# Optimization experiments

Hardware: AMD Instinct MI355X
Metric: run time of the kernel (lower is better)

The kernel has to match this reference:

```python
import jax, jax.numpy as jnp
import numpy as np

N, F, D, R, E = 1024, 256, 64, 11, 2048
ALPHA = 0.2  # LeakyReLU negative slope


def setup_inputs() -> dict:
    key = jax.random.key(0)
    k1, k2, k3, k4, k5, k6 = jax.random.split(key, 6)
    x = jax.random.normal(k1, (N, F), dtype=jnp.float32)
    # Relation-specific weights (ParameterList of [F, D]) stacked: [R, F, D]
    W = jax.random.normal(k2, (R, F, D), dtype=jnp.float32) * (1.414 * (6.0 / (F + D)) ** 0.5)
    # nn.Linear(2*D, 1, bias=False) weight as a vector [2*D]
    a = jax.random.normal(k3, (2 * D,), dtype=jnp.float32) * (1.0 / (2 * D) ** 0.5)
    src_idx = jax.random.randint(k4, (E,), 0, N, dtype=jnp.int32)
    dst_idx = jax.random.randint(k5, (E,), 0, N, dtype=jnp.int32)
    rel_idx = jax.random.randint(k6, (E,), 0, R, dtype=jnp.int32)
    return {"x": x, "W": W, "a": a, "src_idx": src_idx, "dst_idx": dst_idx, "rel_idx": rel_idx}


def reference(x, W, a, src_idx, dst_idx, rel_idx):
    # Per-edge relation weight gather: [E, F, D]
    We = W[rel_idx]
    # einsum('i,ij->ij', emb, W) == row-wise scaling of W by the embedding
    nt = x[dst_idx][:, :, None] * We          # neighbour_temp: [E, F, D]
    ft = x[src_idx][:, :, None] * We          # feature_temp:   [E, F, D]
    hh = jnp.concatenate([ft, nt], axis=-1)   # [E, F, 2D]
    # linear(2D -> 1, no bias) then LeakyReLU: [E, F]
    e = jax.nn.leaky_relu(jnp.einsum('efd,d->ef', hh, a), ALPHA)
    # original: attn = softmax over edge dim (dim=1 of [F, E]); here edges are axis 0
    attn = jax.nn.softmax(e, axis=0)          # [E, F]
    # h[e] = attn[:, e, None] * nt[e]; cat over edges along dim=1 then sum over F
    # => per edge: sum_F attn[e, f] * nt[e, f, :] -> [E, D], flattened to [E*D]
    out = jnp.einsum('ef,efd->ed', attn, nt).reshape(-1)
    return out
```

## Files before the change

### kernel.cpp

```cpp
#include <hip/hip_runtime.h>
#include <hip/hip_bf16.h>

#define NN 1024
#define FF 256
#define DD 64
#define RR 11
#define EE 2048
#define ALPHA 0.2f
#define TPB 512
#define EPT (EE / TPB)
#define TILE_E 32
#define PERM_CAP 2432
#define K2_GRID (PERM_CAP / TILE_E)


__global__ __launch_bounds__(TPB) void k1_coef(
    const float* __restrict__ x, const float* __restrict__ W,
    const float* __restrict__ a, const int* __restrict__ src,
    const int* __restrict__ dst, const int* __restrict__ rel,
    float* __restrict__ cbuf, int* __restrict__ perm,
    int* __restrict__ ntiles_p) {

    const int b    = blockIdx.x;
    const int f    = ((b & 7) << 5) | (b >> 3);
    const int tid  = threadIdx.x;
    const int wid  = tid >> 6;
    const int lane = tid & 63;

    __shared__ float xcol[NN];
    __shared__ float p_sh[RR], q_sh[RR];
    __shared__ float red_s[8];
    __shared__ int   hist[16], off_sh[16];

    for (int i = tid; i < NN; i += TPB) xcol[i] = x[(size_t)i * FF + f];

    for (int r = wid; r < RR; r += 8) {
        float w  = W[((size_t)r * FF + f) * DD + lane];
        float pa = w * a[lane];
        float qa = w * a[DD + lane];
        #pragma unroll
        for (int o = 32; o > 0; o >>= 1) {
            pa += __shfl_down(pa, o);
            qa += __shfl_down(qa, o);
        }
        if (lane == 0) { p_sh[r] = pa; q_sh[r] = qa; }
    }
    __syncthreads();

    float uvals[EPT];
    float s = 0.0f;
    #pragma unroll
    for (int k = 0; k < EPT; ++k) {
        int e = tid + k * TPB;
        float xs = xcol[src[e]];
        float xd = xcol[dst[e]];
        int r = rel[e];
        float v = xs * p_sh[r] + xd * q_sh[r];
        v = v > 0.0f ? v : ALPHA * v;
        float ev = expf(v);
        uvals[k] = ev * xd;
        s += ev;
    }
    #pragma unroll
    for (int o = 32; o > 0; o >>= 1) s += __shfl_down(s, o);
    if (lane == 0) red_s[wid] = s;
    __syncthreads();
    float st = red_s[0];
    #pragma unroll
    for (int i = 1; i < 8; ++i) st += red_s[i];
    float inv = 1.0f / st;

    #pragma unroll
    for (int k = 0; k < EPT; ++k) {
        int e = tid + k * TPB;
        cbuf[(size_t)e * FF + f] = uvals[k] * inv;
    }

    if (b == 0) {
        if (tid < 16) hist[tid] = 0;
        __syncthreads();
        for (int e = tid; e < EE; e += TPB) atomicAdd(&hist[rel[e]], 1);
        __syncthreads();
        if (tid == 0) {
            int acc = 0;
            for (int r = 0; r < RR; ++r) {
                off_sh[r] = acc;
                acc += (hist[r] + TILE_E - 1) & ~(TILE_E - 1);
            }
            *ntiles_p = acc / TILE_E;
        }
        __syncthreads();
        for (int i = tid; i < PERM_CAP; i += TPB) perm[i] = -1;
        __syncthreads();
        for (int e = tid; e < EE; e += TPB) {
            int pos = atomicAdd(&off_sh[rel[e]], 1);
            perm[pos] = e;
        }
    }
}

__global__ __launch_bounds__(TPB) void k2_out(
    const float* __restrict__ W, const int* __restrict__ rel,
    const float* __restrict__ cbuf, const int* __restrict__ perm,
    const int* __restrict__ ntiles_p, float* __restrict__ out) {

    const int t = blockIdx.x;
    if (t >= *ntiles_p) return;

    const int tid  = threadIdx.x;
    const int wid  = tid >> 6;
    const int lane = tid & 63;

    __shared__ float Wl[32 * DD];
    __shared__ int   e_sh[TILE_E];

    if (tid < TILE_E) e_sh[tid] = perm[t * TILE_E + tid];
    __syncthreads();

    const int r = rel[e_sh[0]];
    const float* __restrict__ Wr = W + (size_t)r * FF * DD;

    int eb[4];
    const float* ce[4];
    float4 acc[4];
    #pragma unroll
    for (int j = 0; j < 4; ++j) {
        eb[j]  = e_sh[wid * 4 + j];
        ce[j]  = cbuf + (size_t)(eb[j] >= 0 ? eb[j] : 0) * FF;
        acc[j] = make_float4(0.f, 0.f, 0.f, 0.f);
    }

    const int fg = lane >> 4;
    const int dq = lane & 15;
    const int srow = tid >> 4;
    const int scol = tid & 15;

    float4 nxt = *(const float4*)&Wr[(size_t)srow * DD + scol * 4];

    #pragma unroll
    for (int fc = 0; fc < FF / 32; ++fc) {
        __syncthreads();
        *(float4*)&Wl[srow * DD + scol * 4] = nxt;
        __syncthreads();
        if (fc < FF / 32 - 1)
            nxt = *(const float4*)
                &Wr[(size_t)((fc + 1) * 32 + srow) * DD + scol * 4];
        #pragma unroll
        for (int i = 0; i < 8; ++i) {
            int lf = i * 4 + fg;
            float4 w4 = *(const float4*)&Wl[lf * DD + dq * 4];
            int gf = fc * 32 + lf;
            #pragma unroll
            for (int j = 0; j < 4; ++j) {
                float c = ce[j][gf];
                acc[j].x = fmaf(c, w4.x, acc[j].x);
                acc[j].y = fmaf(c, w4.y, acc[j].y);
                acc[j].z = fmaf(c, w4.z, acc[j].z);
                acc[j].w = fmaf(c, w4.w, acc[j].w);
            }
        }
    }

    #pragma unroll
    for (int j = 0; j < 4; ++j) {
        #pragma unroll
        for (int o = 16; o <= 32; o <<= 1) {
            acc[j].x += __shfl_xor(acc[j].x, o);
            acc[j].y += __shfl_xor(acc[j].y, o);
            acc[j].z += __shfl_xor(acc[j].z, o);
            acc[j].w += __shfl_xor(acc[j].w, o);
        }
        if (eb[j] >= 0 && fg == 0)
            *(float4*)&out[(size_t)eb[j] * DD + dq * 4] = acc[j];
    }
}

extern "C" void kernel_launch(void* const* d_in, const int* in_sizes, int n_in,
                              void* d_out, int out_size, void* d_ws, size_t ws_size,
                              hipStream_t stream) {
    const float* x  = (const float*)d_in[0];
    const float* W  = (const float*)d_in[1];
    const float* a  = (const float*)d_in[2];
    const int* src  = (const int*)d_in[3];
    const int* dst  = (const int*)d_in[4];
    const int* rel  = (const int*)d_in[5];
    float* out      = (float*)d_out;

    char* wsb = (char*)d_ws;
    int*   ntiles_p = (int*)wsb;
    int*   perm     = (int*)(wsb + 256);
    float* cbuf     = (float*)(wsb + 16384);

    k1_coef<<<FF, TPB, 0, stream>>>(x, W, a, src, dst, rel,
                                    cbuf, perm, ntiles_p);
    k2_out<<<K2_GRID, TPB, 0, stream>>>(W, rel, cbuf, perm, ntiles_p, out);
}
```

Baseline: 21.68 us.

## Process four features per block in coefficient kernel and split perm build into own block

Each k1 block now handles four adjacent feature columns, loading x rows as float4 and reusing the src/dst/rel indices held in registers across all four. The permutation-building work moves from block 0 into a dedicated extra block so it no longer delays one compute block. The aim is to cut redundant index loads and strided gathers of x. In exchange the grid shrinks from 256 to 65 blocks on a GPU with many CUs, which lowers parallelism.

Result: slower. 25.95 us (+19.7%).

```diff
diff --git a/kernel.cpp b/kernel.cpp
--- a/kernel.cpp
+++ b/kernel.cpp
@@ -9,6 +9,8 @@
 #define ALPHA 0.2f
 #define TPB 512
 #define EPT (EE / TPB)
+#define FB 4
+#define K1_GRID (FF / FB + 1)
 #define TILE_E 32
 #define PERM_CAP 2432
 #define K2_GRID (PERM_CAP / TILE_E)
@@ -22,61 +24,13 @@
     int* __restrict__ ntiles_p) {
 
     const int b    = blockIdx.x;
-    const int f    = ((b & 7) << 5) | (b >> 3);
     const int tid  = threadIdx.x;
     const int wid  = tid >> 6;
     const int lane = tid & 63;
 
-    __shared__ float xcol[NN];
-    __shared__ float p_sh[RR], q_sh[RR];
-    __shared__ float red_s[8];
-    __shared__ int   hist[16], off_sh[16];
-
-    for (int i = tid; i < NN; i += TPB) xcol[i] = x[(size_t)i * FF + f];
-
-    for (int r = wid; r < RR; r += 8) {
-        float w  = W[((size_t)r * FF + f) * DD + lane];
-        float pa = w * a[lane];
-        float qa = w * a[DD + lane];
-        #pragma unroll
-        for (int o = 32; o > 0; o >>= 1) {
-            pa += __shfl_down(pa, o);
-            qa += __shfl_down(qa, o);
-        }
-        if (lane == 0) { p_sh[r] = pa; q_sh[r] = qa; }
-    }
-    __syncthreads();
-
-    float uvals[EPT];
-    float s = 0.0f;
-    #pragma unroll
-    for (int k = 0; k < EPT; ++k) {
-        int e = tid + k * TPB;
-        float xs = xcol[src[e]];
-        float xd = xcol[dst[e]];
-        int r = rel[e];
-        float v = xs * p_sh[r] + xd * q_sh[r];
-        v = v > 0.0f ? v : ALPHA * v;
-        float ev = expf(v);
-        uvals[k] = ev * xd;
-        s += ev;
-    }
-    #pragma unroll
-    for (int o = 32; o > 0; o >>= 1) s += __shfl_down(s, o);
-    if (lane == 0) red_s[wid] = s;
-    __syncthreads();
-    float st = red_s[0];
-    #pragma unroll
-    for (int i = 1; i < 8; ++i) st += red_s[i];
-    float inv = 1.0f / st;
-
-    #pragma unroll
-    for (int k = 0; k < EPT; ++k) {
-        int e = tid + k * TPB;
-        cbuf[(size_t)e * FF + f] = uvals[k] * inv;
-    }
-
-    if (b == 0) {
+    __shared__ int hist[16], off_sh[16];
+
+    if (b == FF / FB) {
         if (tid < 16) hist[tid] = 0;
         __syncthreads();
         for (int e = tid; e < EE; e += TPB) atomicAdd(&hist[rel[e]], 1);
@@ -95,6 +49,71 @@
         for (int e = tid; e < EE; e += TPB) {
             int pos = atomicAdd(&off_sh[rel[e]], 1);
             perm[pos] = e;
+        }
+        return;
+    }
+
+    const int f0 = (((b & 7) << 3) | (b >> 3)) * FB;
+
+    __shared__ float xs[FB][NN];
+    __shared__ float p_sh[FB][RR], q_sh[FB][RR];
+    __shared__ float red_s[8];
+
+    #pragma unroll
+    for (int i = 0; i < NN / TPB; ++i) {
+        int row = tid + i * TPB;
+        float4 v = *(const float4*)&x[(size_t)row * FF + f0];
+        xs[0][row] = v.x; xs[1][row] = v.y; xs[2][row] = v.z; xs[3][row] = v.w;
+    }
+
+    for (int task = wid; task < FB * RR; task += 8) {
+        int ff = task & (FB - 1), r = task >> 2;
+        float wv = W[((size_t)r * FF + f0 + ff) * DD + lane];
+        float pa = wv * a[lane];
+        float qa = wv * a[DD + lane];
+        #pragma unroll
+        for (int o = 32; o > 0; o >>= 1) {
+            pa += __shfl_down(pa, o);
+            qa += __shfl_down(qa, o);
+        }
+        if (lane == 0) { p_sh[ff][r] = pa; q_sh[ff][r] = qa; }
+    }
+    __syncthreads();
+
+    int siA[EPT], diA[EPT], rA[EPT];
+    #pragma unroll
+    for (int k = 0; k < EPT; ++k) {
+        int e = tid + k * TPB;
+        siA[k] = src[e]; diA[k] = dst[e]; rA[k] = rel[e];
+    }
+
+    for (int ff = 0; ff < FB; ++ff) {
+        float uvals[EPT];
+        float s = 0.0f;
+        #pragma unroll
+        for (int k = 0; k < EPT; ++k) {
+            float xsv = xs[ff][siA[k]];
+            float xdd = xs[ff][diA[k]];
+            float v = xsv * p_sh[ff][rA[k]] + xdd * q_sh[ff][rA[k]];
+            v = v > 0.0f ? v : ALPHA * v;
+            float ev = expf(v);
+            uvals[k] = ev * xdd;
+            s += ev;
+        }
+        #pragma unroll
+        for (int o = 32; o > 0; o >>= 1) s += __shfl_down(s, o);
+        if (lane == 0) red_s[wid] = s;
+        __syncthreads();
+        float st = red_s[0];
+        #pragma unroll
+        for (int i = 1; i < 8; ++i) st += red_s[i];
+        __syncthreads();
+        float inv = 1.0f / st;
+
+        #pragma unroll
+        for (int k = 0; k < EPT; ++k) {
+            int e = tid + k * TPB;
+            cbuf[(size_t)e * FF + f0 + ff] = uvals[k] * inv;
         }
     }
 }
@@ -191,7 +210,7 @@
     int*   perm     = (int*)(wsb + 256);
     float* cbuf     = (float*)(wsb + 16384);
 
-    k1_coef<<<FF, TPB, 0, stream>>>(x, W, a, src, dst, rel,
-                                    cbuf, perm, ntiles_p);
+    k1_coef<<<K1_GRID, TPB, 0, stream>>>(x, W, a, src, dst, rel,
+                                         cbuf, perm, ntiles_p);
     k2_out<<<K2_GRID, TPB, 0, stream>>>(W, rel, cbuf, perm, ntiles_p, out);
 }
```
